# Kernel optimization log

Measured on AMD Instinct MI355X. Metric: run time of the kernel, lower is better.

The kernel has to match this reference:

```python
import jax, jax.numpy as jnp
import numpy as np

N_NODES = 50000
N_EDGES = 800000
NUM_GRAPHS = 512
IN_DIM = 128
HID = 128
OUT_DIM = 1


def setup_inputs() -> dict:
    key = jax.random.key(0)
    ks = jax.random.split(key, 8)
    x = jax.random.normal(ks[0], (N_NODES, IN_DIM), dtype=jnp.float32)
    edge_index = jax.random.randint(ks[1], (2, N_EDGES), 0, N_NODES, dtype=jnp.int64)
    batch = jnp.sort(jax.random.randint(ks[2], (N_NODES,), 0, NUM_GRAPHS, dtype=jnp.int64))
    s1 = 1.0 / np.sqrt(IN_DIM)
    s2 = 1.0 / np.sqrt(HID)
    W1 = jax.random.normal(ks[3], (IN_DIM, HID), dtype=jnp.float32) * s1
    b1 = jnp.zeros((HID,), dtype=jnp.float32)
    W2 = jax.random.normal(ks[4], (HID, HID), dtype=jnp.float32) * s2
    b2 = jnp.zeros((HID,), dtype=jnp.float32)
    Wl = jax.random.normal(ks[5], (HID, OUT_DIM), dtype=jnp.float32) * s2
    bl = jnp.zeros((OUT_DIM,), dtype=jnp.float32)
    return {"x": x, "edge_index": edge_index, "batch": batch,
            "W1": W1, "b1": b1, "W2": W2, "b2": b2, "Wl": Wl, "bl": bl}


def _gcn_conv(x, src, dst, norm, W, b):
    # GCNConv: D^{-1/2}(A+I)D^{-1/2} X W + b (self-loops already in src/dst)
    h = x @ W                                    # [N, H]
    msg = h[src] * norm[:, None]                 # gather + edge-normalize
    agg = jax.ops.segment_sum(msg, dst, num_segments=N_NODES)  # scatter-add
    return agg + b


def reference(x, edge_index, batch, W1, b1, W2, b2, Wl, bl):
    loops = jnp.arange(N_NODES, dtype=edge_index.dtype)
    src = jnp.concatenate([edge_index[0], loops])
    dst = jnp.concatenate([edge_index[1], loops])
    deg = jax.ops.segment_sum(jnp.ones_like(dst, dtype=x.dtype), dst, num_segments=N_NODES)
    dinv = jax.lax.rsqrt(deg)                    # deg >= 1 due to self-loops
    norm = dinv[src] * dinv[dst]                 # symmetric normalization per edge

    h = jax.nn.relu(_gcn_conv(x, src, dst, norm, W1, b1))
    h = jax.nn.relu(_gcn_conv(h, src, dst, norm, W2, b2))

    # global_mean_pool over graph ids
    sums = jax.ops.segment_sum(h, batch, num_segments=NUM_GRAPHS)
    cnts = jax.ops.segment_sum(jnp.ones((N_NODES,), dtype=h.dtype), batch, num_segments=NUM_GRAPHS)
    pooled = sums / jnp.maximum(cnts, 1.0)[:, None]

    out = jax.nn.sigmoid(pooled @ Wl + bl)       # [G, 1]
    return out.squeeze(1)                        # [G]
```

## Files before the change

kernel.cpp:

```cpp
#include <hip/hip_runtime.h>
#include <hip/hip_bf16.h>

#define N_NODES 50000
#define N_EDGES 800000
#define NUM_GRAPHS 512
#define MAXDEG 64
#define EPB 4096
#define P1_BLOCKS 196
#define NBUCK 256
#define NPB 196
#define XCONV_BLOCKS 3125

typedef short short8 __attribute__((ext_vector_type(8)));
typedef unsigned short u16x8 __attribute__((ext_vector_type(8)));
typedef float f32x4 __attribute__((ext_vector_type(4)));

__device__ __forceinline__ unsigned short f2bu(float f) {
    __hip_bfloat16 h = __float2bfloat16(f);
    return *reinterpret_cast<unsigned short*>(&h);
}
__device__ __forceinline__ float bu2f(unsigned short u) {
    unsigned int v = ((unsigned int)u) << 16;
    float f;
    __builtin_memcpy(&f, &v, 4);
    return f;
}

__global__ __launch_bounds__(256) void bin_k(const int* __restrict__ ei,
                                             const float* __restrict__ x,
                                             unsigned int* __restrict__ staging,
                                             int* __restrict__ cnts_tbl,
                                             int* __restrict__ offs_tbl,
                                             unsigned short* __restrict__ xb,
                                             unsigned short* __restrict__ h1,
                                             float* __restrict__ dinv) {
    int b = blockIdx.x, t = threadIdx.x;
    if (b >= P1_BLOCKS) {
        int xi = b - P1_BLOCKS;
        if (xi == 0 && t < 64)
            ((unsigned int*)(xb + (size_t)N_NODES * 128))[t] = 0u;
        if (xi == 1 && t < 64)
            ((unsigned int*)(h1 + (size_t)N_NODES * 128))[t] = 0u;
        if (xi == 2 && t == 0) dinv[N_NODES] = 0.f;
        const float* xp = x + (size_t)xi * 2048 + t * 8;
        float4 v0 = *(const float4*)xp;
        float4 v1 = *(const float4*)(xp + 4);
        u16x8 o;
        o[0] = f2bu(v0.x); o[1] = f2bu(v0.y); o[2] = f2bu(v0.z); o[3] = f2bu(v0.w);
        o[4] = f2bu(v1.x); o[5] = f2bu(v1.y); o[6] = f2bu(v1.z); o[7] = f2bu(v1.w);
        *(u16x8*)(xb + (size_t)xi * 2048 + t * 8) = o;
        return;
    }

    __shared__ unsigned int st[EPB];
    __shared__ int cnt[NBUCK], cur[NBUCK], scan[NBUCK];
    cnt[t] = 0;
    __syncthreads();

    int e0 = b * EPB;
    int srcv[16], dstv[16], bk[16];
#pragma unroll
    for (int k = 0; k < 16; ++k) {
        int e = e0 + k * 256 + t;
        bool ok = e < N_EDGES;
        srcv[k] = ok ? ei[e] : 0;
        dstv[k] = ok ? ei[N_EDGES + e] : 0;
        bk[k] = ok ? (dstv[k] / NPB) : -1;
        if (ok) atomicAdd(&cnt[bk[k]], 1);
    }
    __syncthreads();
    scan[t] = cnt[t];
    __syncthreads();
    for (int off = 1; off < 256; off <<= 1) {
        int u = t >= off ? scan[t - off] : 0;
        __syncthreads();
        scan[t] += u;
        __syncthreads();
    }
    int excl = scan[t] - cnt[t];
    cur[t] = excl;
    cnts_tbl[t * P1_BLOCKS + b] = cnt[t];
    offs_tbl[t * P1_BLOCKS + b] = excl;
    __syncthreads();
#pragma unroll
    for (int k = 0; k < 16; ++k) {
        if (bk[k] >= 0) {
            int pos = atomicAdd(&cur[bk[k]], 1);
            int dl = dstv[k] - bk[k] * NPB;
            st[pos] = (unsigned int)srcv[k] | ((unsigned int)dl << 16);
        }
    }
    __syncthreads();
    unsigned int* gout = staging + (size_t)b * EPB;
    for (int i = t; i < EPB; i += 256) gout[i] = st[i];
}

__global__ __launch_bounds__(256) void adjbuild_k(const unsigned int* __restrict__ staging,
                                                  const int* __restrict__ cnts_tbl,
                                                  const int* __restrict__ offs_tbl,
                                                  unsigned short* __restrict__ adj,
                                                  int* __restrict__ cnt,
                                                  float* __restrict__ dinv,
                                                  const float* __restrict__ W1,
                                                  const float* __restrict__ W2,
                                                  unsigned short* __restrict__ W1t,
                                                  unsigned short* __restrict__ W2t) {
    int b = blockIdx.x, t = threadIdx.x;
    if (b >= NBUCK) {
        int wb = b - NBUCK;
        const float* W = wb < 64 ? W1 : W2;
        unsigned short* Wt = wb < 64 ? W1t : W2t;
        int idx = (wb & 63) * 256 + t;
        int k = idx >> 7, n = idx & 127;
        Wt[n * 128 + k] = f2bu(W[idx]);
        return;
    }
    __shared__ unsigned short adjL[NPB * MAXDEG];
    __shared__ int cntL[NPB];
    __shared__ int segStart[P1_BLOCKS + 1];
    __shared__ int segOff[P1_BLOCKS];
    __shared__ int tmp[256];

    if (t < NPB) cntL[t] = 0;
    int c = t < P1_BLOCKS ? cnts_tbl[b * P1_BLOCKS + t] : 0;
    if (t < P1_BLOCKS) segOff[t] = offs_tbl[b * P1_BLOCKS + t];
    tmp[t] = c;
    __syncthreads();
    for (int off = 1; off < 256; off <<= 1) {
        int u = t >= off ? tmp[t - off] : 0;
        __syncthreads();
        tmp[t] += u;
        __syncthreads();
    }
    if (t < P1_BLOCKS) segStart[t] = tmp[t] - c;
    if (t == 0) segStart[P1_BLOCKS] = tmp[P1_BLOCKS - 1];
    __syncthreads();

    int T = segStart[P1_BLOCKS];
    for (int f = t; f < T; f += 256) {
        int lo = 0, hi = P1_BLOCKS;
        while (hi - lo > 1) {
            int m = (lo + hi) >> 1;
            if (segStart[m] <= f) lo = m; else hi = m;
        }
        unsigned int p = staging[(size_t)lo * EPB + segOff[lo] + (f - segStart[lo])];
        int src = p & 0xFFFF;
        int dl = p >> 16;
        int slot = atomicAdd(&cntL[dl], 1);
        if (slot < MAXDEG - 1) adjL[dl * MAXDEG + slot] = (unsigned short)src;
    }
    __syncthreads();

    int nodeBase = b * NPB;
    if (t < NPB) {
        int node = nodeBase + t;
        int cc = cntL[t];
        int ec = cc < MAXDEG - 1 ? cc : MAXDEG - 1;
        adjL[t * MAXDEG + ec] = (unsigned short)node;
        int tot = ec + 1, tot4 = (tot + 3) & ~3;
        for (int s = tot; s < tot4; ++s) adjL[t * MAXDEG + s] = (unsigned short)N_NODES;
        if (node < N_NODES) {
            cnt[node] = tot4;
            dinv[node] = rsqrtf((float)cc + 1.0f);
        }
    }
    __syncthreads();
    unsigned int* g = (unsigned int*)(adj + (size_t)nodeBase * MAXDEG);
    const unsigned int* l = (const unsigned int*)adjL;
    for (int i = t; i < NPB * MAXDEG / 2; i += 256) g[i] = l[i];
}

__global__ __launch_bounds__(256) void agg1_fused_k(const unsigned short* __restrict__ xb,
                                                    const unsigned short* __restrict__ adj,
                                                    const int* __restrict__ cnt,
                                                    const float* __restrict__ dinv,
                                                    const float* __restrict__ bias,
                                                    const unsigned short* __restrict__ W1t,
                                                    unsigned short* __restrict__ out) {
    __shared__ unsigned short Az[16][136];
    int t = threadIdx.x;
    int wave = t >> 6, lane = t & 63, quad = lane >> 4, fl = lane & 15;
    int nl = wave * 4 + quad;
    int node = blockIdx.x * 16 + nl;
    int2 pack = ((const int2*)(adj + (size_t)node * MAXDEG))[fl];
    int rounds = cnt[node] >> 2;
    float dv = dinv[node];
    int qb = quad << 4;

    float a[8];
#pragma unroll
    for (int j = 0; j < 8; ++j) a[j] = 0.f;

    int i = 0;
    for (; i + 2 <= rounds; i += 2) {
        unsigned pAx = (unsigned)__shfl(pack.x, qb + i, 64);
        unsigned pAy = (unsigned)__shfl(pack.y, qb + i, 64);
        unsigned pBx = (unsigned)__shfl(pack.x, qb + i + 1, 64);
        unsigned pBy = (unsigned)__shfl(pack.y, qb + i + 1, 64);
        unsigned s0 = pAx & 0xFFFFu, s1 = pAx >> 16;
        unsigned s2 = pAy & 0xFFFFu, s3 = pAy >> 16;
        unsigned s4 = pBx & 0xFFFFu, s5 = pBx >> 16;
        unsigned s6 = pBy & 0xFFFFu, s7 = pBy >> 16;
        float d0 = dinv[s0], d1 = dinv[s1], d2 = dinv[s2], d3 = dinv[s3];
        float d4 = dinv[s4], d5 = dinv[s5], d6 = dinv[s6], d7 = dinv[s7];
        u16x8 v0 = *(const u16x8*)(xb + (size_t)s0 * 128 + fl * 8);
        u16x8 v1 = *(const u16x8*)(xb + (size_t)s1 * 128 + fl * 8);
        u16x8 v2 = *(const u16x8*)(xb + (size_t)s2 * 128 + fl * 8);
        u16x8 v3 = *(const u16x8*)(xb + (size_t)s3 * 128 + fl * 8);
        u16x8 v4 = *(const u16x8*)(xb + (size_t)s4 * 128 + fl * 8);
        u16x8 v5 = *(const u16x8*)(xb + (size_t)s5 * 128 + fl * 8);
        u16x8 v6 = *(const u16x8*)(xb + (size_t)s6 * 128 + fl * 8);
        u16x8 v7 = *(const u16x8*)(xb + (size_t)s7 * 128 + fl * 8);
#pragma unroll
        for (int j = 0; j < 8; ++j) {
            a[j] = fmaf(d0, bu2f(v0[j]), a[j]);
            a[j] = fmaf(d1, bu2f(v1[j]), a[j]);
            a[j] = fmaf(d2, bu2f(v2[j]), a[j]);
            a[j] = fmaf(d3, bu2f(v3[j]), a[j]);
            a[j] = fmaf(d4, bu2f(v4[j]), a[j]);
            a[j] = fmaf(d5, bu2f(v5[j]), a[j]);
            a[j] = fmaf(d6, bu2f(v6[j]), a[j]);
            a[j] = fmaf(d7, bu2f(v7[j]), a[j]);
        }
    }
    if (i < rounds) {
        unsigned px = (unsigned)__shfl(pack.x, qb + i, 64);
        unsigned py = (unsigned)__shfl(pack.y, qb + i, 64);
        unsigned s0 = px & 0xFFFFu, s1 = px >> 16;
        unsigned s2 = py & 0xFFFFu, s3 = py >> 16;
        float d0 = dinv[s0], d1 = dinv[s1], d2 = dinv[s2], d3 = dinv[s3];
        u16x8 v0 = *(const u16x8*)(xb + (size_t)s0 * 128 + fl * 8);
        u16x8 v1 = *(const u16x8*)(xb + (size_t)s1 * 128 + fl * 8);
        u16x8 v2 = *(const u16x8*)(xb + (size_t)s2 * 128 + fl * 8);
        u16x8 v3 = *(const u16x8*)(xb + (size_t)s3 * 128 + fl * 8);
#pragma unroll
        for (int j = 0; j < 8; ++j) {
            a[j] = fmaf(d0, bu2f(v0[j]), a[j]);
            a[j] = fmaf(d1, bu2f(v1[j]), a[j]);
            a[j] = fmaf(d2, bu2f(v2[j]), a[j]);
            a[j] = fmaf(d3, bu2f(v3[j]), a[j]);
        }
    }

    u16x8 zv;
#pragma unroll
    for (int j = 0; j < 8; ++j) zv[j] = f2bu(a[j] * dv);
    *(u16x8*)(&Az[nl][fl * 8]) = zv;
    __syncthreads();

    short8 af[4];
#pragma unroll
    for (int ks = 0; ks < 4; ++ks)
        af[ks] = *(const short8*)(&Az[fl][ks * 32 + quad * 8]);

    f32x4 acc[2];
    acc[0] = (f32x4){0.f, 0.f, 0.f, 0.f};
    acc[1] = (f32x4){0.f, 0.f, 0.f, 0.f};
#pragma unroll
    for (int ks = 0; ks < 4; ++ks)
#pragma unroll
        for (int ct = 0; ct < 2; ++ct) {
            short8 b = *(const short8*)(W1t + (size_t)(wave * 32 + ct * 16 + fl) * 128 + ks * 32 + quad * 8);
            acc[ct] = __builtin_amdgcn_mfma_f32_16x16x32_bf16(af[ks], b, acc[ct], 0, 0, 0);
        }

    int colbase = wave * 32;
    float bias0 = bias[colbase + fl];
    float bias1 = bias[colbase + 16 + fl];
    int rowbase = blockIdx.x * 16 + quad * 4;
#pragma unroll
    for (int rr = 0; rr < 4; ++rr) {
        float dvr = dinv[rowbase + rr];
        out[(size_t)(rowbase + rr) * 128 + colbase + fl] =
            f2bu(fmaxf(acc[0][rr] + bias0, 0.f) * dvr);
        out[(size_t)(rowbase + rr) * 128 + colbase + 16 + fl] =
            f2bu(fmaxf(acc[1][rr] + bias1, 0.f) * dvr);
    }
}

__global__ __launch_bounds__(256) void agg2_fused_k(const unsigned short* __restrict__ hs,
                                                    const unsigned short* __restrict__ adj,
                                                    const int* __restrict__ cnt,
                                                    const float* __restrict__ dinv,
                                                    const float* __restrict__ bias,
                                                    const unsigned short* __restrict__ W2t,
                                                    const float* __restrict__ Wl,
                                                    float* __restrict__ pnode) {
    __shared__ unsigned short Az[16][136];
    __shared__ float part[4][16];
    int t = threadIdx.x;
    int wave = t >> 6, lane = t & 63, quad = lane >> 4, fl = lane & 15;
    int nl = wave * 4 + quad;
    int node = blockIdx.x * 16 + nl;
    int2 pack = ((const int2*)(adj + (size_t)node * MAXDEG))[fl];
    int rounds = cnt[node] >> 2;
    float dv = dinv[node];
    int qb = quad << 4;

    float a[8];
#pragma unroll
    for (int j = 0; j < 8; ++j) a[j] = 0.f;

    int i = 0;
    for (; i + 2 <= rounds; i += 2) {
        unsigned pAx = (unsigned)__shfl(pack.x, qb + i, 64);
        unsigned pAy = (unsigned)__shfl(pack.y, qb + i, 64);
        unsigned pBx = (unsigned)__shfl(pack.x, qb + i + 1, 64);
        unsigned pBy = (unsigned)__shfl(pack.y, qb + i + 1, 64);
        u16x8 v0 = *(const u16x8*)(hs + (size_t)(pAx & 0xFFFFu) * 128 + fl * 8);
        u16x8 v1 = *(const u16x8*)(hs + (size_t)(pAx >> 16) * 128 + fl * 8);
        u16x8 v2 = *(const u16x8*)(hs + (size_t)(pAy & 0xFFFFu) * 128 + fl * 8);
        u16x8 v3 = *(const u16x8*)(hs + (size_t)(pAy >> 16) * 128 + fl * 8);
        u16x8 v4 = *(const u16x8*)(hs + (size_t)(pBx & 0xFFFFu) * 128 + fl * 8);
        u16x8 v5 = *(const u16x8*)(hs + (size_t)(pBx >> 16) * 128 + fl * 8);
        u16x8 v6 = *(const u16x8*)(hs + (size_t)(pBy & 0xFFFFu) * 128 + fl * 8);
        u16x8 v7 = *(const u16x8*)(hs + (size_t)(pBy >> 16) * 128 + fl * 8);
#pragma unroll
        for (int j = 0; j < 8; ++j)
            a[j] += ((bu2f(v0[j]) + bu2f(v1[j])) + (bu2f(v2[j]) + bu2f(v3[j])))
                  + ((bu2f(v4[j]) + bu2f(v5[j])) + (bu2f(v6[j]) + bu2f(v7[j])));
    }
    if (i < rounds) {
        unsigned px = (unsigned)__shfl(pack.x, qb + i, 64);
        unsigned py = (unsigned)__shfl(pack.y, qb + i, 64);
        u16x8 v0 = *(const u16x8*)(hs + (size_t)(px & 0xFFFFu) * 128 + fl * 8);
        u16x8 v1 = *(const u16x8*)(hs + (size_t)(px >> 16) * 128 + fl * 8);
        u16x8 v2 = *(const u16x8*)(hs + (size_t)(py & 0xFFFFu) * 128 + fl * 8);
        u16x8 v3 = *(const u16x8*)(hs + (size_t)(py >> 16) * 128 + fl * 8);
#pragma unroll
        for (int j = 0; j < 8; ++j)
            a[j] += (bu2f(v0[j]) + bu2f(v1[j])) + (bu2f(v2[j]) + bu2f(v3[j]));
    }

    u16x8 zv;
#pragma unroll
    for (int j = 0; j < 8; ++j) zv[j] = f2bu(a[j] * dv);
    *(u16x8*)(&Az[nl][fl * 8]) = zv;
    __syncthreads();

    short8 af[4];
#pragma unroll
    for (int ks = 0; ks < 4; ++ks)
        af[ks] = *(const short8*)(&Az[fl][ks * 32 + quad * 8]);

    f32x4 acc[2];
    acc[0] = (f32x4){0.f, 0.f, 0.f, 0.f};
    acc[1] = (f32x4){0.f, 0.f, 0.f, 0.f};
#pragma unroll
    for (int ks = 0; ks < 4; ++ks)
#pragma unroll
        for (int ct = 0; ct < 2; ++ct) {
            short8 b = *(const short8*)(W2t + (size_t)(wave * 32 + ct * 16 + fl) * 128 + ks * 32 + quad * 8);
            acc[ct] = __builtin_amdgcn_mfma_f32_16x16x32_bf16(af[ks], b, acc[ct], 0, 0, 0);
        }

    float p[4];
#pragma unroll
    for (int rr = 0; rr < 4; ++rr) {
        float s = 0.f;
#pragma unroll
        for (int ct = 0; ct < 2; ++ct) {
            int col = wave * 32 + ct * 16 + fl;
            s += fmaxf(acc[ct][rr] + bias[col], 0.f) * Wl[col];
        }
        p[rr] = s;
    }
#pragma unroll
    for (int rr = 0; rr < 4; ++rr) {
        p[rr] += __shfl_xor(p[rr], 1, 64);
        p[rr] += __shfl_xor(p[rr], 2, 64);
        p[rr] += __shfl_xor(p[rr], 4, 64);
        p[rr] += __shfl_xor(p[rr], 8, 64);
    }
    if (fl == 0) {
#pragma unroll
        for (int rr = 0; rr < 4; ++rr) part[wave][quad * 4 + rr] = p[rr];
    }
    __syncthreads();
    if (t < 16)
        pnode[blockIdx.x * 16 + t] = part[0][t] + part[1][t] + part[2][t] + part[3][t];
}

__device__ __forceinline__ int lb(const int* a, int n, int v) {
    int lo = 0, hi = n;
    while (lo < hi) {
        int m = (lo + hi) >> 1;
        if (a[m] < v) lo = m + 1;
        else hi = m;
    }
    return lo;
}

__global__ __launch_bounds__(64) void final_k(const float* __restrict__ pnode,
                                              const int* __restrict__ batch,
                                              const float* __restrict__ bl,
                                              float* __restrict__ out) {
    int g = blockIdx.x, t = threadIdx.x;
    int lo = lb(batch, N_NODES, g), hi = lb(batch, N_NODES, g + 1);
    float s = 0.f;
    for (int r = lo + t; r < hi; r += 64) s += pnode[r];
#pragma unroll
    for (int o = 32; o > 0; o >>= 1) s += __shfl_down(s, o, 64);
    if (t == 0) {
        float cf = (float)(hi - lo);
        float z = s / fmaxf(cf, 1.f) + bl[0];
        out[g] = 1.f / (1.f + expf(-z));
    }
}

extern "C" void kernel_launch(void* const* d_in, const int* in_sizes, int n_in,
                              void* d_out, int out_size, void* d_ws, size_t ws_size,
                              hipStream_t stream) {
    const float* x = (const float*)d_in[0];
    const int* ei = (const int*)d_in[1];
    const int* batch = (const int*)d_in[2];
    const float* W1 = (const float*)d_in[3];
    const float* b1 = (const float*)d_in[4];
    const float* W2 = (const float*)d_in[5];
    const float* b2 = (const float*)d_in[6];
    const float* Wl = (const float*)d_in[7];
    const float* bl = (const float*)d_in[8];
    float* out = (float*)d_out;

    char* ws = (char*)d_ws;
    unsigned int* staging = (unsigned int*)(ws + 0x0);
    int* cnts_tbl = (int*)(ws + 0x310000);
    int* offs_tbl = (int*)(ws + 0x341000);
    unsigned short* adj = (unsigned short*)(ws + 0x372000);
    int* cnt = (int*)(ws + 0x992000);
    float* dinv = (float*)(ws + 0x9C3000);
    unsigned short* W1t = (unsigned short*)(ws + 0x9F4000);
    unsigned short* W2t = (unsigned short*)(ws + 0x9FC000);
    float* pnode = (float*)(ws + 0xA04000);
    unsigned short* xb = (unsigned short*)(ws + 0xA36000);
    unsigned short* h1 = (unsigned short*)(ws + 0x1672000);

    bin_k<<<P1_BLOCKS + XCONV_BLOCKS, 256, 0, stream>>>(ei, x, staging, cnts_tbl,
                                                        offs_tbl, xb, h1, dinv);
    adjbuild_k<<<NBUCK + 128, 256, 0, stream>>>(staging, cnts_tbl, offs_tbl,
                                                adj, cnt, dinv, W1, W2, W1t, W2t);
    agg1_fused_k<<<N_NODES / 16, 256, 0, stream>>>(xb, adj, cnt, dinv, b1, W1t, h1);
    agg2_fused_k<<<N_NODES / 16, 256, 0, stream>>>(h1, adj, cnt, dinv, b2, W2t, Wl, pnode);
    final_k<<<NUM_GRAPHS, 64, 0, stream>>>(pnode, batch, bl, out);
}
```

Measured before the change: 188.0 us.

## Replace two-pass binned CSR build with global atomic scatter and staged stores

```diff
diff --git a/kernel.cpp b/kernel.cpp
--- a/kernel.cpp
+++ b/kernel.cpp
@@ -5,11 +5,10 @@
 #define N_EDGES 800000
 #define NUM_GRAPHS 512
 #define MAXDEG 64
-#define EPB 4096
-#define P1_BLOCKS 196
-#define NBUCK 256
-#define NPB 196
 #define XCONV_BLOCKS 3125
+#define WT_BLOCKS 128
+#define ZC_BLOCKS 49
+#define SETUP_BLOCKS (XCONV_BLOCKS + WT_BLOCKS + ZC_BLOCKS)
 
 typedef short short8 __attribute__((ext_vector_type(8)));
 typedef unsigned short u16x8 __attribute__((ext_vector_type(8)));
@@ -26,17 +25,18 @@
     return f;
 }
 
-__global__ __launch_bounds__(256) void bin_k(const int* __restrict__ ei,
-                                             const float* __restrict__ x,
-                                             unsigned int* __restrict__ staging,
-                                             int* __restrict__ cnts_tbl,
-                                             int* __restrict__ offs_tbl,
-                                             unsigned short* __restrict__ xb,
-                                             unsigned short* __restrict__ h1,
-                                             float* __restrict__ dinv) {
+__global__ __launch_bounds__(256) void setup_k(const float* __restrict__ x,
+                                               unsigned short* __restrict__ xb,
+                                               unsigned short* __restrict__ h1,
+                                               float* __restrict__ dinv,
+                                               int* __restrict__ cnt,
+                                               const float* __restrict__ W1,
+                                               const float* __restrict__ W2,
+                                               unsigned short* __restrict__ W1t,
+                                               unsigned short* __restrict__ W2t) {
     int b = blockIdx.x, t = threadIdx.x;
-    if (b >= P1_BLOCKS) {
-        int xi = b - P1_BLOCKS;
+    if (b < XCONV_BLOCKS) {
+        int xi = b;
         if (xi == 0 && t < 64)
             ((unsigned int*)(xb + (size_t)N_NODES * 128))[t] = 0u;
         if (xi == 1 && t < 64)
@@ -51,63 +51,8 @@
         *(u16x8*)(xb + (size_t)xi * 2048 + t * 8) = o;
         return;
     }
-
-    __shared__ unsigned int st[EPB];
-    __shared__ int cnt[NBUCK], cur[NBUCK], scan[NBUCK];
-    cnt[t] = 0;
-    __syncthreads();
-
-    int e0 = b * EPB;
-    int srcv[16], dstv[16], bk[16];
-#pragma unroll
-    for (int k = 0; k < 16; ++k) {
-        int e = e0 + k * 256 + t;
-        bool ok = e < N_EDGES;
-        srcv[k] = ok ? ei[e] : 0;
-        dstv[k] = ok ? ei[N_EDGES + e] : 0;
-        bk[k] = ok ? (dstv[k] / NPB) : -1;
-        if (ok) atomicAdd(&cnt[bk[k]], 1);
-    }
-    __syncthreads();
-    scan[t] = cnt[t];
-    __syncthreads();
-    for (int off = 1; off < 256; off <<= 1) {
-        int u = t >= off ? scan[t - off] : 0;
-        __syncthreads();
-        scan[t] += u;
-        __syncthreads();
-    }
-    int excl = scan[t] - cnt[t];
-    cur[t] = excl;
-    cnts_tbl[t * P1_BLOCKS + b] = cnt[t];
-    offs_tbl[t * P1_BLOCKS + b] = excl;
-    __syncthreads();
-#pragma unroll
-    for (int k = 0; k < 16; ++k) {
-        if (bk[k] >= 0) {
-            int pos = atomicAdd(&cur[bk[k]], 1);
-            int dl = dstv[k] - bk[k] * NPB;
-            st[pos] = (unsigned int)srcv[k] | ((unsigned int)dl << 16);
-        }
-    }
-    __syncthreads();
-    unsigned int* gout = staging + (size_t)b * EPB;
-    for (int i = t; i < EPB; i += 256) gout[i] = st[i];
-}
-
-__global__ __launch_bounds__(256) void adjbuild_k(const unsigned int* __restrict__ staging,
-                                                  const int* __restrict__ cnts_tbl,
-                                                  const int* __restrict__ offs_tbl,
-                                                  unsigned short* __restrict__ adj,
-                                                  int* __restrict__ cnt,
-                                                  float* __restrict__ dinv,
-                                                  const float* __restrict__ W1,
-                                                  const float* __restrict__ W2,
-                                                  unsigned short* __restrict__ W1t,
-                                                  unsigned short* __restrict__ W2t) {
-    int b = blockIdx.x, t = threadIdx.x;
-    if (b >= NBUCK) {
-        int wb = b - NBUCK;
+    if (b < XCONV_BLOCKS + WT_BLOCKS) {
+        int wb = b - XCONV_BLOCKS;
         const float* W = wb < 64 ? W1 : W2;
         unsigned short* Wt = wb < 64 ? W1t : W2t;
         int idx = (wb & 63) * 256 + t;
@@ -115,59 +60,39 @@
         Wt[n * 128 + k] = f2bu(W[idx]);
         return;
     }
-    __shared__ unsigned short adjL[NPB * MAXDEG];
-    __shared__ int cntL[NPB];
-    __shared__ int segStart[P1_BLOCKS + 1];
-    __shared__ int segOff[P1_BLOCKS];
-    __shared__ int tmp[256];
-
-    if (t < NPB) cntL[t] = 0;
-    int c = t < P1_BLOCKS ? cnts_tbl[b * P1_BLOCKS + t] : 0;
-    if (t < P1_BLOCKS) segOff[t] = offs_tbl[b * P1_BLOCKS + t];
-    tmp[t] = c;
-    __syncthreads();
-    for (int off = 1; off < 256; off <<= 1) {
-        int u = t >= off ? tmp[t - off] : 0;
-        __syncthreads();
-        tmp[t] += u;
-        __syncthreads();
-    }
-    if (t < P1_BLOCKS) segStart[t] = tmp[t] - c;
-    if (t == 0) segStart[P1_BLOCKS] = tmp[P1_BLOCKS - 1];
-    __syncthreads();
-
-    int T = segStart[P1_BLOCKS];
-    for (int f = t; f < T; f += 256) {
-        int lo = 0, hi = P1_BLOCKS;
-        while (hi - lo > 1) {
-            int m = (lo + hi) >> 1;
-            if (segStart[m] <= f) lo = m; else hi = m;
-        }
-        unsigned int p = staging[(size_t)lo * EPB + segOff[lo] + (f - segStart[lo])];
-        int src = p & 0xFFFF;
-        int dl = p >> 16;
-        int slot = atomicAdd(&cntL[dl], 1);
-        if (slot < MAXDEG - 1) adjL[dl * MAXDEG + slot] = (unsigned short)src;
-    }
-    __syncthreads();
-
-    int nodeBase = b * NPB;
-    if (t < NPB) {
-        int node = nodeBase + t;
-        int cc = cntL[t];
-        int ec = cc < MAXDEG - 1 ? cc : MAXDEG - 1;
-        adjL[t * MAXDEG + ec] = (unsigned short)node;
-        int tot = ec + 1, tot4 = (tot + 3) & ~3;
-        for (int s = tot; s < tot4; ++s) adjL[t * MAXDEG + s] = (unsigned short)N_NODES;
-        if (node < N_NODES) {
-            cnt[node] = tot4;
-            dinv[node] = rsqrtf((float)cc + 1.0f);
-        }
-    }
-    __syncthreads();
-    unsigned int* g = (unsigned int*)(adj + (size_t)nodeBase * MAXDEG);
-    const unsigned int* l = (const unsigned int*)adjL;
-    for (int i = t; i < NPB * MAXDEG / 2; i += 256) g[i] = l[i];
+    int zi = (b - XCONV_BLOCKS - WT_BLOCKS) * 1024 + t * 4;
+    *(int4*)(cnt + zi) = (int4){0, 0, 0, 0};
+}
+
+__global__ __launch_bounds__(256) void scatter_k(const int* __restrict__ ei,
+                                                 int* __restrict__ cnt,
+                                                 unsigned short* __restrict__ adj) {
+    int t = threadIdx.x, b = blockIdx.x;
+    int e0 = b * 1024 + t;
+#pragma unroll
+    for (int k = 0; k < 4; ++k) {
+        int e = e0 + k * 256;
+        if (e < N_EDGES) {
+            int src = ei[e];
+            int dst = ei[N_EDGES + e];
+            int pos = atomicAdd(&cnt[dst], 1);
+            if (pos < MAXDEG - 1) adj[(size_t)dst * MAXDEG + pos] = (unsigned short)src;
+        }
+    }
+}
+
+__global__ __launch_bounds__(256) void finalize_k(unsigned short* __restrict__ adj,
+                                                  int* __restrict__ cnt,
+                                                  float* __restrict__ dinv) {
+    int node = blockIdx.x * 256 + threadIdx.x;
+    if (node >= N_NODES) return;
+    int cc = cnt[node];
+    int ec = cc < MAXDEG - 1 ? cc : MAXDEG - 1;
+    adj[(size_t)node * MAXDEG + ec] = (unsigned short)node;
+    int tot = ec + 1, tot4 = (tot + 3) & ~3;
+    for (int s = tot; s < tot4; ++s) adj[(size_t)node * MAXDEG + s] = (unsigned short)N_NODES;
+    cnt[node] = tot4;
+    dinv[node] = rsqrtf((float)cc + 1.0f);
 }
 
 __global__ __launch_bounds__(256) void agg1_fused_k(const unsigned short* __restrict__ xb,
@@ -264,18 +189,21 @@
             acc[ct] = __builtin_amdgcn_mfma_f32_16x16x32_bf16(af[ks], b, acc[ct], 0, 0, 0);
         }
 
+    __syncthreads();
     int colbase = wave * 32;
     float bias0 = bias[colbase + fl];
     float bias1 = bias[colbase + 16 + fl];
-    int rowbase = blockIdx.x * 16 + quad * 4;
+    int rowq = quad * 4;
 #pragma unroll
     for (int rr = 0; rr < 4; ++rr) {
-        float dvr = dinv[rowbase + rr];
-        out[(size_t)(rowbase + rr) * 128 + colbase + fl] =
-            f2bu(fmaxf(acc[0][rr] + bias0, 0.f) * dvr);
-        out[(size_t)(rowbase + rr) * 128 + colbase + 16 + fl] =
-            f2bu(fmaxf(acc[1][rr] + bias1, 0.f) * dvr);
-    }
+        float dvr = dinv[blockIdx.x * 16 + rowq + rr];
+        Az[rowq + rr][colbase + fl]      = f2bu(fmaxf(acc[0][rr] + bias0, 0.f) * dvr);
+        Az[rowq + rr][colbase + 16 + fl] = f2bu(fmaxf(acc[1][rr] + bias1, 0.f) * dvr);
+    }
+    __syncthreads();
+    int row = t >> 4, c8 = t & 15;
+    *(u16x8*)(out + (size_t)(blockIdx.x * 16 + row) * 128 + c8 * 8) =
+        *(const u16x8*)(&Az[row][c8 * 8]);
 }
 
 __global__ __launch_bounds__(256) void agg2_fused_k(const unsigned short* __restrict__ hs,
@@ -423,9 +351,6 @@
     float* out = (float*)d_out;
 
     char* ws = (char*)d_ws;
-    unsigned int* staging = (unsigned int*)(ws + 0x0);
-    int* cnts_tbl = (int*)(ws + 0x310000);
-    int* offs_tbl = (int*)(ws + 0x341000);
     unsigned short* adj = (unsigned short*)(ws + 0x372000);
     int* cnt = (int*)(ws + 0x992000);
     float* dinv = (float*)(ws + 0x9C3000);
@@ -435,10 +360,9 @@
     unsigned short* xb = (unsigned short*)(ws + 0xA36000);
     unsigned short* h1 = (unsigned short*)(ws + 0x1672000);
 
-    bin_k<<<P1_BLOCKS + XCONV_BLOCKS, 256, 0, stream>>>(ei, x, staging, cnts_tbl,
-                                                        offs_tbl, xb, h1, dinv);
-    adjbuild_k<<<NBUCK + 128, 256, 0, stream>>>(staging, cnts_tbl, offs_tbl,
-                                                adj, cnt, dinv, W1, W2, W1t, W2t);
+    setup_k<<<SETUP_BLOCKS, 256, 0, stream>>>(x, xb, h1, dinv, cnt, W1, W2, W1t, W2t);
+    scatter_k<<<(N_EDGES + 1023) / 1024, 256, 0, stream>>>(ei, cnt, adj);
+    finalize_k<<<196, 256, 0, stream>>>(adj, cnt, dinv);
     agg1_fused_k<<<N_NODES / 16, 256, 0, stream>>>(xb, adj, cnt, dinv, b1, W1t, h1);
     agg2_fused_k<<<N_NODES / 16, 256, 0, stream>>>(h1, adj, cnt, dinv, b2, W2t, Wl, pnode);
     final_k<<<NUM_GRAPHS, 64, 0, stream>>>(pnode, batch, bl, out);
```

Result: slower. 221.5 us (+17.8%).
